# Kernel optimization log

Measured on AMD Instinct MI355X. Metric: run time of the kernel, lower is better.

The kernel has to match this reference:

```python
import jax, jax.numpy as jnp
import numpy as np

N_DYADIC = 0   # init kwarg n: dyadic refinement order (0 = no refinement)


def _sig_kernel_gram(X, Y):
    """Signature-kernel Gram matrix via Goursat PDE solve (solver=0, linear kernel).

    X: (A, M, D), Y: (B, N, D). Returns K: (A, B) with K[a,b] = k_sig(x^a, y^b).
    PDE scheme: K[i+1,j+1] = K[i+1,j] + K[i,j+1] + K[i,j]*(inc[i,j] - 1),
    K[0,:] = K[:,0] = 1, inc[i,j] = <x_{i+1}-x_i, y_{j+1}-y_j>.
    The j-recursion is a prefix sum, so each row update is a vectorized cumsum;
    only the i-direction is sequential (lax.scan over M-1 rows).
    """
    dtype = X.dtype
    dX = X[:, 1:, :] - X[:, :-1, :]          # (A, M-1, D)
    dY = Y[:, 1:, :] - Y[:, :-1, :]          # (B, N-1, D)
    inc = jnp.einsum('amd,bnd->abmn', dX, dY)  # (A, B, M-1, N-1) increment grid
    if N_DYADIC > 0:
        f = 2 ** N_DYADIC
        inc = jnp.repeat(jnp.repeat(inc, f, axis=2), f, axis=3) / (f * f)
    A, B, M1, N1 = inc.shape
    ones_col = jnp.ones((A, B, 1), dtype)
    k0 = jnp.ones((A, B, N1 + 1), dtype)      # boundary row K[0, :] = 1

    def step(k_prev, inc_row):
        # k_new[j+1] = k_new[j] + (k_prev[j+1] - k_prev[j] + k_prev[j]*inc[j])
        delta = k_prev[..., 1:] - k_prev[..., :-1] + k_prev[..., :-1] * inc_row
        k_new = jnp.concatenate([ones_col, 1.0 + jnp.cumsum(delta, axis=-1)], axis=-1)
        return k_new, None

    k_last, _ = jax.lax.scan(step, k0, jnp.moveaxis(inc, 2, 0))
    return k_last[..., -1]                    # (A, B): K(s=T, t=T)


def setup_inputs() -> dict:
    key = jax.random.key(0)
    kx, ky = jax.random.split(key)
    # scale 0.1 keeps path increments moderate so the PDE solution stays well-conditioned
    X = jax.random.normal(kx, (64, 128, 64), dtype=jnp.float32) * 0.1
    Y = jax.random.normal(ky, (64, 128, 64), dtype=jnp.float32) * 0.1
    return {"X": X, "Y": Y}


def reference(X, Y):
    K_XX = _sig_kernel_gram(X, X)
    K_YY = _sig_kernel_gram(Y, Y)
    K_XY = _sig_kernel_gram(X, Y)
    dist = jnp.mean(K_XX) + jnp.mean(K_YY) - 2.0 * jnp.mean(K_XY)
    return jnp.mean((X[:, 0, :] - Y[:, 0, :]) ** 2) + dist
```

## Files before the change

kernel.cpp:

```cpp
#include <hip/hip_runtime.h>

#define AA   64
#define MM   128
#define DD   64
#define CSTR 132
#define NXY  512
#define NTRI 288
#define NBLK (NXY + 2*NTRI)
#define REG_I4 65536
#define PART_OFF (4u << 20)

typedef float f32x4 __attribute__((ext_vector_type(4)));
typedef short bf8_t __attribute__((ext_vector_type(8)));

template <int CTRL, int RM>
__device__ __forceinline__ float dpp0(float x) {
    return __int_as_float(
        __builtin_amdgcn_update_dpp(0, __float_as_int(x), CTRL, RM, 0xF, false));
}

__device__ __forceinline__ unsigned bf16_rne(float v) {
    unsigned u = __float_as_uint(v);
    return (u + 0x7FFFu + ((u >> 16) & 1u)) >> 16;
}
__device__ __forceinline__ float bf16_tof(unsigned h) {
    return __uint_as_float(h << 16);
}

__device__ __forceinline__ void lds_fence() {
    asm volatile("s_waitcnt lgkmcnt(0)" ::: "memory");
    __builtin_amdgcn_sched_barrier(0);
}

__global__ __launch_bounds__(256) void prep_frags(const float* __restrict__ X,
                                                  const float* __restrict__ Y,
                                                  int4* __restrict__ frag) {
    const int tid = threadIdx.x, lane = tid & 63, w = tid >> 6;
    const int W    = blockIdx.x * 4 + w;
    const int inp  = W >> 9;
    const int p    = (W >> 3) & 63;
    const int tile = W & 7;
    const float* S = (inp ? Y : X) + p * (MM * DD);
    int i = tile * 16 + (lane & 15);
    if (i > 126) i = 126;
    const int d0 = (lane >> 4) << 3;

    int4* hi = frag + (inp * 2 + 0) * REG_I4;
    int4* lo = frag + (inp * 2 + 1) * REG_I4;
    const int base = p * 1024 + tile * 128 + lane;

    #pragma unroll
    for (int ks = 0; ks < 2; ++ks) {
        const float* r0 = S + i * DD + ks * 32 + d0;
        const float* r1 = r0 + DD;
        float4 a0 = *(const float4*)r0;
        float4 a1 = *(const float4*)(r0 + 4);
        float4 c0 = *(const float4*)r1;
        float4 c1 = *(const float4*)(r1 + 4);
        float v[8] = {c0.x - a0.x, c0.y - a0.y, c0.z - a0.z, c0.w - a0.w,
                      c1.x - a1.x, c1.y - a1.y, c1.z - a1.z, c1.w - a1.w};
        unsigned hs[8], ls[8];
        #pragma unroll
        for (int e = 0; e < 8; ++e) {
            hs[e] = bf16_rne(v[e]);
            ls[e] = bf16_rne(v[e] - bf16_tof(hs[e]));
        }
        int4 h, l;
        h.x = hs[0] | (hs[1] << 16); h.y = hs[2] | (hs[3] << 16);
        h.z = hs[4] | (hs[5] << 16); h.w = hs[6] | (hs[7] << 16);
        l.x = ls[0] | (ls[1] << 16); l.y = ls[2] | (ls[3] << 16);
        l.z = ls[4] | (ls[5] << 16); l.w = ls[6] | (ls[7] << 16);
        hi[base + ks * 64] = h;
        lo[base + ks * 64] = l;
    }
}

template <int ROWS>
__device__ __forceinline__ void load_sv(const float* buf, int c2l, float2* sv) {
    #pragma unroll
    for (int r = 0; r < ROWS; ++r)
        sv[r] = *(const float2*)(buf + r * CSTR + c2l);
}

template <int ROWS>
__device__ __forceinline__ void chain2_sv(const float2* svP, const float2* svQ,
                                          int lane,
                                          float& S0, float& e00, float& e10,
                                          float& S1, float& e01, float& e11) {
    #pragma unroll
    for (int r = 0; r < ROWS; ++r) {
        float s0a = svP[r].x, s1a = (lane < 63) ? svP[r].y : 0.0f;
        float s0b = svQ[r].x, s1b = (lane < 63) ? svQ[r].y : 0.0f;
        float Spa = dpp0<0x138, 0xF>(S0);
        float Spb = dpp0<0x138, 0xF>(S1);
        float k0a = 1.0f + Spa, k1a = 1.0f + S0 - e10;
        float k0b = 1.0f + Spb, k1b = 1.0f + S1 - e11;
        float e0a = fmaf(k0a, s0a, e00), e1a = fmaf(k1a, s1a, e10);
        float e0b = fmaf(k0b, s0b, e01), e1b = fmaf(k1b, s1b, e11);
        float Sa = e0a + e1a;
        float Sb = e0b + e1b;
        Sa += dpp0<0x111, 0xF>(Sa);  Sb += dpp0<0x111, 0xF>(Sb);
        Sa += dpp0<0x112, 0xF>(Sa);  Sb += dpp0<0x112, 0xF>(Sb);
        Sa += dpp0<0x114, 0xF>(Sa);  Sb += dpp0<0x114, 0xF>(Sb);
        Sa += dpp0<0x118, 0xF>(Sa);  Sb += dpp0<0x118, 0xF>(Sb);
        Sa += dpp0<0x142, 0xA>(Sa);  Sb += dpp0<0x142, 0xA>(Sb);
        Sa += dpp0<0x143, 0xC>(Sa);  Sb += dpp0<0x143, 0xC>(Sb);
        S0 = Sa; e00 = e0a; e10 = e1a;
        S1 = Sb; e01 = e0b; e11 = e1b;
    }
}

__global__ __launch_bounds__(256, 2)
void sig_pde(const int4* __restrict__ frag, float* __restrict__ partials) {
    const int tid = threadIdx.x, lane = tid & 63, w = tid >> 6;
    const int gid = blockIdx.x;

    int b, a0, a1, ain, bin;
    float wgt0, wgt1;
    if (gid < NXY) {
        b = gid >> 3;
        int abase = (gid & 7) * 8;
        a0 = abase + 2 * w; a1 = a0 + 1;
        ain = 0; bin = 1;
        wgt0 = wgt1 = -2.0f / 4096.0f;
    } else {
        int t = gid - NXY;
        int inp = 0;
        if (t >= NTRI) { t -= NTRI; inp = 1; }
        int g = (int)((__builtin_sqrtf((float)(t + 1)) - 1.0f) * 0.5f);
        while (4 * (g + 1) * (g + 2) <= t) ++g;
        while (g > 0 && 4 * g * (g + 1) > t) --g;
        int r  = t - 4 * g * (g + 1);
        int bi = r / (g + 1);
        int c  = r - bi * (g + 1);
        b = 8 * g + bi;
        int abase = c * 8;
        a0 = abase + 2 * w; a1 = a0 + 1;
        ain = bin = inp;
        wgt0 = (a0 < b) ? (2.0f / 4096.0f) : ((a0 == b) ? (1.0f / 4096.0f) : 0.0f);
        wgt1 = (a1 < b) ? (2.0f / 4096.0f) : ((a1 == b) ? (1.0f / 4096.0f) : 0.0f);
    }

    __shared__ int4  Bh[1024], Bl[1024];
    __shared__ float incS[8][8 * CSTR];
    __shared__ float red8[8];

    {
        const int4* Bhg = frag + (bin * 2 + 0) * REG_I4 + b * 1024;
        const int4* Blg = frag + (bin * 2 + 1) * REG_I4 + b * 1024;
        #pragma unroll
        for (int c = 0; c < 4; ++c) {
            int idx = c * 256 + tid;
            Bh[idx] = Bhg[idx];
            Bl[idx] = Blg[idx];
        }
    }
    __syncthreads();

    const int4* Ahg0 = frag + (ain * 2 + 0) * REG_I4 + a0 * 1024;
    const int4* Alg0 = frag + (ain * 2 + 1) * REG_I4 + a0 * 1024;
    const int4* Ahg1 = frag + (ain * 2 + 0) * REG_I4 + a1 * 1024;
    const int4* Alg1 = frag + (ain * 2 + 1) * REG_I4 + a1 * 1024;

    int4 A0h[2], A0l[2], A1h[2], A1l[2];
    int4 N0h[2], N0l[2], N1h[2], N1l[2];
    f32x4 acc[2][8];
    float S0 = 0.f, e00 = 0.f, e10 = 0.f;
    float S1 = 0.f, e01 = 0.f, e11 = 0.f;

    float* buf0 = &incS[2 * w + 0][0];
    float* buf1 = &incS[2 * w + 1][0];
    const int c2l = lane << 1;
    const int r0w = (lane >> 4) << 2, c0w = lane & 15;

#define MFMA_PASS() do {                                                        \
    _Pragma("unroll")                                                           \
    for (int p_ = 0; p_ < 2; ++p_)                                              \
        _Pragma("unroll")                                                       \
        for (int t_ = 0; t_ < 8; ++t_) acc[p_][t_] = (f32x4){0.f,0.f,0.f,0.f};  \
    _Pragma("unroll")                                                           \
    for (int s_ = 0; s_ < 2; ++s_) {                                            \
        bf8_t ah0 = __builtin_bit_cast(bf8_t, A0h[s_]);                         \
        bf8_t al0 = __builtin_bit_cast(bf8_t, A0l[s_]);                         \
        bf8_t ah1 = __builtin_bit_cast(bf8_t, A1h[s_]);                         \
        bf8_t al1 = __builtin_bit_cast(bf8_t, A1l[s_]);                         \
        _Pragma("unroll")                                                       \
        for (int t_ = 0; t_ < 8; ++t_) {                                        \
            int fb = (t_ * 2 + s_) * 64 + lane;                                 \
            bf8_t bh = *(const bf8_t*)&Bh[fb];                                  \
            bf8_t bl = *(const bf8_t*)&Bl[fb];                                  \
            acc[0][t_] = __builtin_amdgcn_mfma_f32_16x16x32_bf16(ah0, bh, acc[0][t_], 0, 0, 0); \
            acc[1][t_] = __builtin_amdgcn_mfma_f32_16x16x32_bf16(ah1, bh, acc[1][t_], 0, 0, 0); \
            acc[0][t_] = __builtin_amdgcn_mfma_f32_16x16x32_bf16(ah0, bl, acc[0][t_], 0, 0, 0); \
            acc[1][t_] = __builtin_amdgcn_mfma_f32_16x16x32_bf16(ah1, bl, acc[1][t_], 0, 0, 0); \
            acc[0][t_] = __builtin_amdgcn_mfma_f32_16x16x32_bf16(al0, bh, acc[0][t_], 0, 0, 0); \
            acc[1][t_] = __builtin_amdgcn_mfma_f32_16x16x32_bf16(al1, bh, acc[1][t_], 0, 0, 0); \
        }                                                                       \
    }                                                                           \
} while (0)

#define STORE_H(p, half, buf) do {                             \
    if ((r0w & 8) == ((half) << 3)) {                          \
        float* pb = (buf) + (r0w & 7) * CSTR + c0w;            \
        _Pragma("unroll")                                      \
        for (int t_ = 0; t_ < 8; ++t_) {                       \
            float* q = pb + (t_ << 4);                         \
            q[0]        = acc[p][t_][0];                       \
            q[CSTR]     = acc[p][t_][1];                       \
            q[2 * CSTR] = acc[p][t_][2];                       \
            q[3 * CSTR] = acc[p][t_][3];                       \
        }                                                      \
    }                                                          \
} while (0)

#define LOAD_A_N(poff) do {                                    \
    int off = (poff) + lane;                                   \
    N0h[0] = Ahg0[off]; N0h[1] = Ahg0[off + 64];               \
    N0l[0] = Alg0[off]; N0l[1] = Alg0[off + 64];               \
    N1h[0] = Ahg1[off]; N1h[1] = Ahg1[off + 64];               \
    N1l[0] = Alg1[off]; N1l[1] = Alg1[off + 64];               \
} while (0)

    A0h[0] = Ahg0[lane]; A0h[1] = Ahg0[64 + lane];
    A0l[0] = Alg0[lane]; A0l[1] = Alg0[64 + lane];
    A1h[0] = Ahg1[lane]; A1h[1] = Ahg1[64 + lane];
    A1l[0] = Alg1[lane]; A1l[1] = Alg1[64 + lane];
    MFMA_PASS();

    for (int s = 0; s < 8; ++s) {
        if (s < 7) LOAD_A_N((s + 1) * 128);

        float2 sv00[8], sv10[8];
        lds_fence();
        STORE_H(0, 0, buf0); load_sv<8>(buf0, c2l, sv00);
        STORE_H(1, 0, buf1); load_sv<8>(buf1, c2l, sv10);
        chain2_sv<8>(sv00, sv10, lane, S0, e00, e10, S1, e01, e11);

        lds_fence();
        if (s < 7) {
            float2 sv01[8], sv11[8];
            STORE_H(0, 1, buf0); load_sv<8>(buf0, c2l, sv01);
            STORE_H(1, 1, buf1); load_sv<8>(buf1, c2l, sv11);
            A0h[0] = N0h[0]; A0h[1] = N0h[1]; A0l[0] = N0l[0]; A0l[1] = N0l[1];
            A1h[0] = N1h[0]; A1h[1] = N1h[1]; A1l[0] = N1l[0]; A1l[1] = N1l[1];
            MFMA_PASS();
            chain2_sv<8>(sv01, sv11, lane, S0, e00, e10, S1, e01, e11);
        } else {
            float2 sv01[7], sv11[7];
            STORE_H(0, 1, buf0); load_sv<7>(buf0, c2l, sv01);
            STORE_H(1, 1, buf1); load_sv<7>(buf1, c2l, sv11);
            chain2_sv<7>(sv01, sv11, lane, S0, e00, e10, S1, e01, e11);
        }
    }

    if (lane == 63) {
        red8[2 * w + 0] = wgt0 * (1.0f + S0 - e10);
        red8[2 * w + 1] = wgt1 * (1.0f + S1 - e11);
    }
    __syncthreads();
    if (tid == 0) {
        float r = 0.f;
        #pragma unroll
        for (int i = 0; i < 8; ++i) r += red8[i];
        partials[gid] = r;
    }

#undef MFMA_PASS
#undef STORE_H
#undef LOAD_A_N
}

__global__ void final_sum(const float* __restrict__ X, const float* __restrict__ Y,
                          const float* __restrict__ partials, float* __restrict__ out) {
    __shared__ float red[4];
    int tid = threadIdx.x;
    float acc = 0.f;
    for (int e = tid; e < NBLK; e += 256) acc += partials[e];
    for (int e = tid; e < AA * DD; e += 256) {
        int aa = e >> 6, d = e & 63;
        float df = X[aa * (MM * DD) + d] - Y[aa * (MM * DD) + d];
        acc = fmaf(df * df, 1.0f / 4096.0f, acc);
    }
    #pragma unroll
    for (int off = 32; off > 0; off >>= 1) acc += __shfl_down(acc, off);
    if ((tid & 63) == 0) red[tid >> 6] = acc;
    __syncthreads();
    if (tid == 0) out[0] = red[0] + red[1] + red[2] + red[3];
}

extern "C" void kernel_launch(void* const* d_in, const int* in_sizes, int n_in,
                              void* d_out, int out_size, void* d_ws, size_t ws_size,
                              hipStream_t stream) {
    const float* X = (const float*)d_in[0];
    const float* Y = (const float*)d_in[1];
    float* out = (float*)d_out;
    int4*  frag = (int4*)d_ws;
    float* partials = (float*)((char*)d_ws + PART_OFF);

    hipLaunchKernelGGL(prep_frags, dim3(256), dim3(256), 0, stream, X, Y, frag);
    hipLaunchKernelGGL(sig_pde, dim3(NBLK), dim3(256), 0, stream, frag, partials);
    hipLaunchKernelGGL(final_sum, dim3(1), dim3(256), 0, stream, X, Y, partials, out);
}
```

Before: 165.3 us.

## Shrink LDS staging to quarter tiles and raise occupancy to three blocks

After: 240.7 us. 45.6% more time.

```diff
diff --git a/kernel.cpp b/kernel.cpp
--- a/kernel.cpp
+++ b/kernel.cpp
@@ -17,6 +17,11 @@
 __device__ __forceinline__ float dpp0(float x) {
     return __int_as_float(
         __builtin_amdgcn_update_dpp(0, __float_as_int(x), CTRL, RM, 0xF, false));
+}
+template <int CTRL, int RM>
+__device__ __forceinline__ float dpp1(float x) {
+    return __int_as_float(
+        __builtin_amdgcn_update_dpp(0x3f800000, __float_as_int(x), CTRL, RM, 0xF, false));
 }
 
 __device__ __forceinline__ unsigned bf16_rne(float v) {
@@ -42,6 +47,7 @@
     const int tile = W & 7;
     const float* S = (inp ? Y : X) + p * (MM * DD);
     int i = tile * 16 + (lane & 15);
+    const bool zr = (i > 126);
     if (i > 126) i = 126;
     const int d0 = (lane >> 4) << 3;
 
@@ -62,6 +68,7 @@
         unsigned hs[8], ls[8];
         #pragma unroll
         for (int e = 0; e < 8; ++e) {
+            if (zr) v[e] = 0.0f;
             hs[e] = bf16_rne(v[e]);
             ls[e] = bf16_rne(v[e] - bf16_tof(hs[e]));
         }
@@ -84,19 +91,18 @@
 
 template <int ROWS>
 __device__ __forceinline__ void chain2_sv(const float2* svP, const float2* svQ,
-                                          int lane,
-                                          float& S0, float& e00, float& e10,
-                                          float& S1, float& e01, float& e11) {
+                                          float& T0, float& e00, float& e10,
+                                          float& T1, float& e01, float& e11) {
     #pragma unroll
     for (int r = 0; r < ROWS; ++r) {
-        float s0a = svP[r].x, s1a = (lane < 63) ? svP[r].y : 0.0f;
-        float s0b = svQ[r].x, s1b = (lane < 63) ? svQ[r].y : 0.0f;
-        float Spa = dpp0<0x138, 0xF>(S0);
-        float Spb = dpp0<0x138, 0xF>(S1);
-        float k0a = 1.0f + Spa, k1a = 1.0f + S0 - e10;
-        float k0b = 1.0f + Spb, k1b = 1.0f + S1 - e11;
-        float e0a = fmaf(k0a, s0a, e00), e1a = fmaf(k1a, s1a, e10);
-        float e0b = fmaf(k0b, s0b, e01), e1b = fmaf(k1b, s1b, e11);
+        float k0a = dpp1<0x138, 0xF>(T0);
+        float k0b = dpp1<0x138, 0xF>(T1);
+        float k1a = T0 - e10;
+        float k1b = T1 - e11;
+        float e0a = fmaf(k0a, svP[r].x, e00);
+        float e0b = fmaf(k0b, svQ[r].x, e01);
+        float e1a = fmaf(k1a, svP[r].y, e10);
+        float e1b = fmaf(k1b, svQ[r].y, e11);
         float Sa = e0a + e1a;
         float Sb = e0b + e1b;
         Sa += dpp0<0x111, 0xF>(Sa);  Sb += dpp0<0x111, 0xF>(Sb);
@@ -105,12 +111,13 @@
         Sa += dpp0<0x118, 0xF>(Sa);  Sb += dpp0<0x118, 0xF>(Sb);
         Sa += dpp0<0x142, 0xA>(Sa);  Sb += dpp0<0x142, 0xA>(Sb);
         Sa += dpp0<0x143, 0xC>(Sa);  Sb += dpp0<0x143, 0xC>(Sb);
-        S0 = Sa; e00 = e0a; e10 = e1a;
-        S1 = Sb; e01 = e0b; e11 = e1b;
-    }
-}
-
-__global__ __launch_bounds__(256, 2)
+        T0 = 1.0f + Sa; T1 = 1.0f + Sb;
+        e00 = e0a; e10 = e1a;
+        e01 = e0b; e11 = e1b;
+    }
+}
+
+__global__ __launch_bounds__(256, 3)
 void sig_pde(const int4* __restrict__ frag, float* __restrict__ partials) {
     const int tid = threadIdx.x, lane = tid & 63, w = tid >> 6;
     const int gid = blockIdx.x;
@@ -142,7 +149,7 @@
     }
 
     __shared__ int4  Bh[1024], Bl[1024];
-    __shared__ float incS[8][8 * CSTR];
+    __shared__ float incS[8][4 * CSTR];
     __shared__ float red8[8];
 
     {
@@ -165,13 +172,14 @@
     int4 A0h[2], A0l[2], A1h[2], A1l[2];
     int4 N0h[2], N0l[2], N1h[2], N1l[2];
     f32x4 acc[2][8];
-    float S0 = 0.f, e00 = 0.f, e10 = 0.f;
-    float S1 = 0.f, e01 = 0.f, e11 = 0.f;
+    float T0 = 1.f, e00 = 0.f, e10 = 0.f;
+    float T1 = 1.f, e01 = 0.f, e11 = 0.f;
 
     float* buf0 = &incS[2 * w + 0][0];
     float* buf1 = &incS[2 * w + 1][0];
     const int c2l = lane << 1;
-    const int r0w = (lane >> 4) << 2, c0w = lane & 15;
+    const int qw  = lane >> 4;
+    const int c0w = lane & 15;
 
 #define MFMA_PASS() do {                                                        \
     _Pragma("unroll")                                                           \
@@ -199,16 +207,16 @@
     }                                                                           \
 } while (0)
 
-#define STORE_H(p, half, buf) do {                             \
-    if ((r0w & 8) == ((half) << 3)) {                          \
-        float* pb = (buf) + (r0w & 7) * CSTR + c0w;            \
+#define STORE_Q(p, q, buf) do {                                \
+    if (qw == (q)) {                                           \
+        float* pb = (buf) + c0w;                               \
         _Pragma("unroll")                                      \
         for (int t_ = 0; t_ < 8; ++t_) {                       \
-            float* q = pb + (t_ << 4);                         \
-            q[0]        = acc[p][t_][0];                       \
-            q[CSTR]     = acc[p][t_][1];                       \
-            q[2 * CSTR] = acc[p][t_][2];                       \
-            q[3 * CSTR] = acc[p][t_][3];                       \
+            float* qq = pb + (t_ << 4);                        \
+            qq[0]        = acc[p][t_][0];                      \
+            qq[CSTR]     = acc[p][t_][1];                      \
+            qq[2 * CSTR] = acc[p][t_][2];                      \
+            qq[3 * CSTR] = acc[p][t_][3];                      \
         }                                                      \
     }                                                          \
 } while (0)
@@ -230,32 +238,37 @@
     for (int s = 0; s < 8; ++s) {
         if (s < 7) LOAD_A_N((s + 1) * 128);
 
-        float2 sv00[8], sv10[8];
+        #pragma unroll
+        for (int q = 0; q < 3; ++q) {
+            float2 sv0[4], sv1[4];
+            lds_fence();
+            STORE_Q(0, q, buf0); load_sv<4>(buf0, c2l, sv0);
+            STORE_Q(1, q, buf1); load_sv<4>(buf1, c2l, sv1);
+            chain2_sv<4>(sv0, sv1, T0, e00, e10, T1, e01, e11);
+        }
+
         lds_fence();
-        STORE_H(0, 0, buf0); load_sv<8>(buf0, c2l, sv00);
-        STORE_H(1, 0, buf1); load_sv<8>(buf1, c2l, sv10);
-        chain2_sv<8>(sv00, sv10, lane, S0, e00, e10, S1, e01, e11);
-
-        lds_fence();
+        STORE_Q(0, 3, buf0);
+        STORE_Q(1, 3, buf1);
         if (s < 7) {
-            float2 sv01[8], sv11[8];
-            STORE_H(0, 1, buf0); load_sv<8>(buf0, c2l, sv01);
-            STORE_H(1, 1, buf1); load_sv<8>(buf1, c2l, sv11);
+            float2 sv0[4], sv1[4];
+            load_sv<4>(buf0, c2l, sv0);
+            load_sv<4>(buf1, c2l, sv1);
             A0h[0] = N0h[0]; A0h[1] = N0h[1]; A0l[0] = N0l[0]; A0l[1] = N0l[1];
             A1h[0] = N1h[0]; A1h[1] = N1h[1]; A1l[0] = N1l[0]; A1l[1] = N1l[1];
             MFMA_PASS();
-            chain2_sv<8>(sv01, sv11, lane, S0, e00, e10, S1, e01, e11);
+            chain2_sv<4>(sv0, sv1, T0, e00, e10, T1, e01, e11);
         } else {
-            float2 sv01[7], sv11[7];
-            STORE_H(0, 1, buf0); load_sv<7>(buf0, c2l, sv01);
-            STORE_H(1, 1, buf1); load_sv<7>(buf1, c2l, sv11);
-            chain2_sv<7>(sv01, sv11, lane, S0, e00, e10, S1, e01, e11);
+            float2 sv0[3], sv1[3];
+            load_sv<3>(buf0, c2l, sv0);
+            load_sv<3>(buf1, c2l, sv1);
+            chain2_sv<3>(sv0, sv1, T0, e00, e10, T1, e01, e11);
         }
     }
 
     if (lane == 63) {
-        red8[2 * w + 0] = wgt0 * (1.0f + S0 - e10);
-        red8[2 * w + 1] = wgt1 * (1.0f + S1 - e11);
+        red8[2 * w + 0] = wgt0 * (T0 - e10);
+        red8[2 * w + 1] = wgt1 * (T1 - e11);
     }
     __syncthreads();
     if (tid == 0) {
@@ -266,7 +279,7 @@
     }
 
 #undef MFMA_PASS
-#undef STORE_H
+#undef STORE_Q
 #undef LOAD_A_N
 }
 
```

## Pack two PDE chains per wave, four columns per lane, shorter scan

Applied to the files above, without the earlier changes.

After: 149.3 us. -9.7%, faster.

```diff
diff --git a/kernel.cpp b/kernel.cpp
--- a/kernel.cpp
+++ b/kernel.cpp
@@ -76,37 +76,39 @@
 }
 
 template <int ROWS>
-__device__ __forceinline__ void load_sv(const float* buf, int c2l, float2* sv) {
+__device__ __forceinline__ void load4(const float* buf, int c4, float4* sv) {
     #pragma unroll
     for (int r = 0; r < ROWS; ++r)
-        sv[r] = *(const float2*)(buf + r * CSTR + c2l);
+        sv[r] = *(const float4*)(buf + r * CSTR + c4);
 }
 
 template <int ROWS>
-__device__ __forceinline__ void chain2_sv(const float2* svP, const float2* svQ,
-                                          int lane,
-                                          float& S0, float& e00, float& e10,
-                                          float& S1, float& e01, float& e11) {
+__device__ __forceinline__ void chain4(const float4* sv, bool lq0, bool lq31,
+                                       float& Sv, float& e0p, float& e1p,
+                                       float& e2p, float& e3p) {
     #pragma unroll
     for (int r = 0; r < ROWS; ++r) {
-        float s0a = svP[r].x, s1a = (lane < 63) ? svP[r].y : 0.0f;
-        float s0b = svQ[r].x, s1b = (lane < 63) ? svQ[r].y : 0.0f;
-        float Spa = dpp0<0x138, 0xF>(S0);
-        float Spb = dpp0<0x138, 0xF>(S1);
-        float k0a = 1.0f + Spa, k1a = 1.0f + S0 - e10;
-        float k0b = 1.0f + Spb, k1b = 1.0f + S1 - e11;
-        float e0a = fmaf(k0a, s0a, e00), e1a = fmaf(k1a, s1a, e10);
-        float e0b = fmaf(k0b, s0b, e01), e1b = fmaf(k1b, s1b, e11);
-        float Sa = e0a + e1a;
-        float Sb = e0b + e1b;
-        Sa += dpp0<0x111, 0xF>(Sa);  Sb += dpp0<0x111, 0xF>(Sb);
-        Sa += dpp0<0x112, 0xF>(Sa);  Sb += dpp0<0x112, 0xF>(Sb);
-        Sa += dpp0<0x114, 0xF>(Sa);  Sb += dpp0<0x114, 0xF>(Sb);
-        Sa += dpp0<0x118, 0xF>(Sa);  Sb += dpp0<0x118, 0xF>(Sb);
-        Sa += dpp0<0x142, 0xA>(Sa);  Sb += dpp0<0x142, 0xA>(Sb);
-        Sa += dpp0<0x143, 0xC>(Sa);  Sb += dpp0<0x143, 0xC>(Sb);
-        S0 = Sa; e00 = e0a; e10 = e1a;
-        S1 = Sb; e01 = e0b; e11 = e1b;
+        float s0 = sv[r].x, s1 = sv[r].y, s2 = sv[r].z;
+        float s3 = lq31 ? 0.0f : sv[r].w;
+        float Sp = dpp0<0x138, 0xF>(Sv);
+        Sp = lq0 ? 0.0f : Sp;
+        float t23 = e2p + e3p;
+        float k0 = 1.0f + Sp;
+        float k1 = 1.0f + (Sv - (e1p + t23));
+        float k2 = 1.0f + (Sv - t23);
+        float k3 = 1.0f + (Sv - e3p);
+        float e0 = fmaf(k0, s0, e0p);
+        float e1 = fmaf(k1, s1, e1p);
+        float e2 = fmaf(k2, s2, e2p);
+        float e3 = fmaf(k3, s3, e3p);
+        float E = (e0 + e1) + (e2 + e3);
+        E += dpp0<0x111, 0xF>(E);
+        E += dpp0<0x112, 0xF>(E);
+        E += dpp0<0x114, 0xF>(E);
+        E += dpp0<0x118, 0xF>(E);
+        E += dpp0<0x142, 0xA>(E);
+        Sv = E;
+        e0p = e0; e1p = e1; e2p = e2; e3p = e3;
     }
 }
 
@@ -165,12 +167,14 @@
     int4 A0h[2], A0l[2], A1h[2], A1l[2];
     int4 N0h[2], N0l[2], N1h[2], N1l[2];
     f32x4 acc[2][8];
-    float S0 = 0.f, e00 = 0.f, e10 = 0.f;
-    float S1 = 0.f, e01 = 0.f, e11 = 0.f;
+    float Sv = 0.f, e0p = 0.f, e1p = 0.f, e2p = 0.f, e3p = 0.f;
 
     float* buf0 = &incS[2 * w + 0][0];
     float* buf1 = &incS[2 * w + 1][0];
-    const int c2l = lane << 1;
+    const float* myBuf = (lane < 32) ? buf0 : buf1;
+    const int lq  = lane & 31;
+    const int c4  = lq << 2;
+    const bool lq0 = (lq == 0), lq31 = (lq == 31);
     const int r0w = (lane >> 4) << 2, c0w = lane & 15;
 
 #define MFMA_PASS() do {                                                        \
@@ -221,41 +225,45 @@
     N1l[0] = Alg1[off]; N1l[1] = Alg1[off + 64];               \
 } while (0)
 
-    A0h[0] = Ahg0[lane]; A0h[1] = Ahg0[64 + lane];
-    A0l[0] = Alg0[lane]; A0l[1] = Alg0[64 + lane];
-    A1h[0] = Ahg1[lane]; A1h[1] = Ahg1[64 + lane];
-    A1l[0] = Alg1[lane]; A1l[1] = Alg1[64 + lane];
+    {
+        int off = lane;
+        A0h[0] = Ahg0[off]; A0h[1] = Ahg0[off + 64];
+        A0l[0] = Alg0[off]; A0l[1] = Alg0[off + 64];
+        A1h[0] = Ahg1[off]; A1h[1] = Ahg1[off + 64];
+        A1l[0] = Alg1[off]; A1l[1] = Alg1[off + 64];
+    }
     MFMA_PASS();
 
     for (int s = 0; s < 8; ++s) {
         if (s < 7) LOAD_A_N((s + 1) * 128);
 
-        float2 sv00[8], sv10[8];
+        float4 svA[8];
         lds_fence();
-        STORE_H(0, 0, buf0); load_sv<8>(buf0, c2l, sv00);
-        STORE_H(1, 0, buf1); load_sv<8>(buf1, c2l, sv10);
-        chain2_sv<8>(sv00, sv10, lane, S0, e00, e10, S1, e01, e11);
+        STORE_H(0, 0, buf0);
+        STORE_H(1, 0, buf1);
+        load4<8>(myBuf, c4, svA);
+        chain4<8>(svA, lq0, lq31, Sv, e0p, e1p, e2p, e3p);
 
         lds_fence();
+        STORE_H(0, 1, buf0);
+        STORE_H(1, 1, buf1);
         if (s < 7) {
-            float2 sv01[8], sv11[8];
-            STORE_H(0, 1, buf0); load_sv<8>(buf0, c2l, sv01);
-            STORE_H(1, 1, buf1); load_sv<8>(buf1, c2l, sv11);
+            float4 svB[8];
+            load4<8>(myBuf, c4, svB);
             A0h[0] = N0h[0]; A0h[1] = N0h[1]; A0l[0] = N0l[0]; A0l[1] = N0l[1];
             A1h[0] = N1h[0]; A1h[1] = N1h[1]; A1l[0] = N1l[0]; A1l[1] = N1l[1];
             MFMA_PASS();
-            chain2_sv<8>(sv01, sv11, lane, S0, e00, e10, S1, e01, e11);
+            chain4<8>(svB, lq0, lq31, Sv, e0p, e1p, e2p, e3p);
         } else {
-            float2 sv01[7], sv11[7];
-            STORE_H(0, 1, buf0); load_sv<7>(buf0, c2l, sv01);
-            STORE_H(1, 1, buf1); load_sv<7>(buf1, c2l, sv11);
-            chain2_sv<7>(sv01, sv11, lane, S0, e00, e10, S1, e01, e11);
+            float4 svB[7];
+            load4<7>(myBuf, c4, svB);
+            chain4<7>(svB, lq0, lq31, Sv, e0p, e1p, e2p, e3p);
         }
     }
 
-    if (lane == 63) {
-        red8[2 * w + 0] = wgt0 * (1.0f + S0 - e10);
-        red8[2 * w + 1] = wgt1 * (1.0f + S1 - e11);
+    if (lq == 31) {
+        float wgt = (lane < 32) ? wgt0 : wgt1;
+        red8[2 * w + (lane >> 5)] = wgt * (1.0f + Sv - e3p);
     }
     __syncthreads();
     if (tid == 0) {
```
